# Optimization experiments

Hardware: AMD Instinct MI355X
Metric: run time of the kernel (lower is better)

Reference implementation:

```python
import jax, jax.numpy as jnp
import numpy as np

B, D, H = 65536, 3, 256  # collocation batch, coord dim, hidden width


def setup_inputs() -> dict:
    key = jax.random.key(0)
    ks = jax.random.split(key, 8)

    def init(k, shape, fan_in):
        return jax.random.normal(k, shape, dtype=jnp.float32) * np.float32(1.0 / np.sqrt(fan_in))

    return {
        "x": jax.random.uniform(ks[0], (B, D), dtype=jnp.float32, minval=0.1, maxval=1.0),
        "W0": init(ks[1], (D, H), D), "b0": jnp.zeros((H,), jnp.float32),
        "W1": init(ks[2], (H, H), H), "b1": jnp.zeros((H,), jnp.float32),
        "W2": init(ks[3], (H, H), H), "b2": jnp.zeros((H,), jnp.float32),
        "W3": init(ks[4], (H, H), H), "b3": jnp.zeros((H,), jnp.float32),
        "Wout": init(ks[5], (H, 1), H), "bout": jnp.zeros((1,), jnp.float32),
    }


def reference(x, W0, b0, W1, b1, W2, b2, W3, b3, Wout, bout):
    # Scalar PINN network u(xi), xi: [D]
    def u_fn(xi):
        h = jnp.tanh(xi @ W0 + b0)
        h = jnp.tanh(h @ W1 + b1)
        h = jnp.tanh(h @ W2 + b2)
        h = jnp.tanh(h @ W3 + b3)
        return (h @ Wout + bout)[0]

    u = jax.vmap(u_fn)(x)                               # [B]
    # batch_gradient: du/dx_i for every coordinate axis (Cartesian: no adjustment)
    grads = jax.vmap(jax.grad(u_fn))(x)                 # [B, D]
    # batch_hessian diagonal: d^2u/dx_i^2 via forward-over-reverse
    hess_fn = jax.jacfwd(jax.grad(u_fn))                # [D, D] per sample
    hess_diag = jax.vmap(lambda xi: jnp.diagonal(hess_fn(xi)))(x)  # [B, D]
    # pack (u, grad, hessian-diagonal) as the PDE-residual ingredients
    return jnp.concatenate([u[:, None], grads, hess_diag], axis=1)  # [B, 1+D+D]
```

## Files before the change

kernel.cpp:

```cpp
#include <hip/hip_runtime.h>
#include <hip/hip_fp16.h>

#define HDIM 256
#define MS 16
#define LDAK 264
#define CSTRIDE (MS * LDAK * 2)

typedef _Float16 half8 __attribute__((ext_vector_type(8)));
typedef _Float16 half4 __attribute__((ext_vector_type(4)));
typedef _Float16 half2v __attribute__((ext_vector_type(2)));
typedef float f32x4 __attribute__((ext_vector_type(4)));

__device__ __forceinline__ float fast_tanh(float x) {
    float e = __expf(2.0f * x);
    return 1.0f - 2.0f * __builtin_amdgcn_rcpf(e + 1.0f);
}

__device__ __forceinline__ half4 cvt4(float a, float b, float c, float d) {
    half2v lo = __builtin_bit_cast(half2v, __builtin_amdgcn_cvt_pkrtz(a, b));
    half2v hi = __builtin_bit_cast(half2v, __builtin_amdgcn_cvt_pkrtz(c, d));
    half4 r; r[0] = lo[0]; r[1] = lo[1]; r[2] = hi[0]; r[3] = hi[1];
    return r;
}

__device__ __forceinline__ void barrier_lds() {
    asm volatile("s_waitcnt lgkmcnt(0)\n\ts_barrier" ::: "memory");
}

__global__ __launch_bounds__(256) void pack_weights(const float* __restrict__ W1,
                                                    const float* __restrict__ W2,
                                                    const float* __restrict__ W3,
                                                    _Float16* __restrict__ out) {
    int tid = blockIdx.x * 256 + threadIdx.x;
    int l = tid >> 13;
    int idx = tid & 8191;
    int kg = idx >> 8;
    int n = idx & 255;
    const float* W = (l == 0) ? W1 : (l == 1) ? W2 : W3;
    half8 v;
    #pragma unroll
    for (int j = 0; j < 8; ++j) v[j] = (_Float16)W[(kg * 8 + j) * 256 + n];
    *(half8*)(out + l * 65536 + kg * 2048 + n * 8) = v;
}

__global__ __launch_bounds__(256, 2)
void pinn_fused(const float* __restrict__ x,
                const float* __restrict__ W0,
                const float* __restrict__ b0,
                const float* __restrict__ b1,
                const float* __restrict__ b2,
                const float* __restrict__ b3,
                const float* __restrict__ Wout,
                const float* __restrict__ bout,
                const _Float16* __restrict__ Wp,
                float* __restrict__ out) {
    __shared__ __align__(16) _Float16 Abuf[7 * MS][LDAK];
    __shared__ float part[4 * 7 * MS];

    const int tid  = threadIdx.x;
    const int lane = tid & 63;
    const int wid  = tid >> 6;
    const int qd   = lane >> 4;
    const int n15  = lane & 15;
    const int base = blockIdx.x * MS;
    const int nw   = wid * 64 + n15;

    const int voff0 = (qd * 256 + nw) * 8;

    const char* Ab = (const char*)Abuf;
    const int abase = (n15 * LDAK + qd * 8) * 2;
    char* Sb = (char*)Abuf;
    const int sbase = (n15 * LDAK + wid * 64 + qd * 4) * 2;

    const int perm[8] = {0, 2, 4, 6, 1, 3, 5, 7};

    half8 wf[3][4];

#define PREF(J) do { \
    if ((J) < 24) { \
        const int gp_ = (((J) >> 3) * 8) + perm[(J) & 7]; \
        _Pragma("unroll") \
        for (int t_ = 0; t_ < 4; ++t_) \
            wf[(J) % 3][t_] = *(const half8*)(Wp + gp_ * 8192 + voff0 + t_ * 128); \
    } \
} while (0)

#define KSTEP(ACC, J) do { \
    const int s_ = perm[(J) & 7]; \
    PREF((J) + 2); \
    half8 af_[7]; \
    _Pragma("unroll") \
    for (int c_ = 0; c_ < 7; ++c_) \
        af_[c_] = *(const half8*)(Ab + abase + c_ * CSTRIDE + s_ * 64); \
    _Pragma("unroll") \
    for (int c_ = 0; c_ < 7; ++c_) \
        _Pragma("unroll") \
        for (int t_ = 0; t_ < 4; ++t_) \
            ACC[c_][t_] = __builtin_amdgcn_mfma_f32_16x16x32_f16(wf[(J) % 3][t_], af_[c_], ACC[c_][t_], 0, 0, 0); \
} while (0)

#define ELEMW(ACC, BB, T) do { \
    const int ncol_ = wid * 64 + (T) * 16 + qd * 4; \
    f32x4 bv_ = *(const f32x4*)((BB) + ncol_); \
    float tv_[4], gj_[3][4], sj_[3][4]; \
    _Pragma("unroll") \
    for (int r_ = 0; r_ < 4; ++r_) { \
        float zv_ = ACC[0][T][r_] + bv_[r_]; \
        tv_[r_] = fast_tanh(zv_); \
        float dd_ = 1.f - tv_[r_] * tv_[r_]; \
        float c2_ = -2.f * tv_[r_] * dd_; \
        _Pragma("unroll") \
        for (int i_ = 0; i_ < 3; ++i_) { \
            float zg_ = ACC[1 + i_][T][r_]; \
            float zs_ = ACC[4 + i_][T][r_]; \
            gj_[i_][r_] = dd_ * zg_; \
            sj_[i_][r_] = dd_ * zs_ + c2_ * zg_ * zg_; \
        } \
    } \
    *(half4*)(Sb + sbase + 0 * CSTRIDE + (T) * 32) = cvt4(tv_[0], tv_[1], tv_[2], tv_[3]); \
    _Pragma("unroll") \
    for (int i_ = 0; i_ < 3; ++i_) { \
        *(half4*)(Sb + sbase + (1 + i_) * CSTRIDE + (T) * 32) = \
            cvt4(gj_[i_][0], gj_[i_][1], gj_[i_][2], gj_[i_][3]); \
        *(half4*)(Sb + sbase + (4 + i_) * CSTRIDE + (T) * 32) = \
            cvt4(sj_[i_][0], sj_[i_][1], sj_[i_][2], sj_[i_][3]); \
    } \
} while (0)

#define L0CHUNK(N0) do { \
    const int n0_ = (N0); \
    f32x4 w0v_[2], w1v_[2], w2v_[2], b0v_[2]; \
    w0v_[0] = *(const f32x4*)(W0 + n0_);            w0v_[1] = *(const f32x4*)(W0 + n0_ + 4); \
    w1v_[0] = *(const f32x4*)(W0 + HDIM + n0_);     w1v_[1] = *(const f32x4*)(W0 + HDIM + n0_ + 4); \
    w2v_[0] = *(const f32x4*)(W0 + 2 * HDIM + n0_); w2v_[1] = *(const f32x4*)(W0 + 2 * HDIM + n0_ + 4); \
    b0v_[0] = *(const f32x4*)(b0 + n0_);            b0v_[1] = *(const f32x4*)(b0 + n0_ + 4); \
    half8 h_[7]; \
    _Pragma("unroll") \
    for (int r_ = 0; r_ < 8; ++r_) { \
        const float w0_ = w0v_[r_ >> 2][r_ & 3]; \
        const float w1_ = w1v_[r_ >> 2][r_ & 3]; \
        const float w2_ = w2v_[r_ >> 2][r_ & 3]; \
        float z_  = x0 * w0_ + x1 * w1_ + x2 * w2_ + b0v_[r_ >> 2][r_ & 3]; \
        float tv_ = fast_tanh(z_); \
        float dd_ = 1.f - tv_ * tv_; \
        float c2_ = -2.f * tv_ * dd_; \
        h_[0][r_] = (_Float16)tv_; \
        h_[1][r_] = (_Float16)(dd_ * w0_); \
        h_[2][r_] = (_Float16)(dd_ * w1_); \
        h_[3][r_] = (_Float16)(dd_ * w2_); \
        h_[4][r_] = (_Float16)(c2_ * w0_ * w0_); \
        h_[5][r_] = (_Float16)(c2_ * w1_ * w1_); \
        h_[6][r_] = (_Float16)(c2_ * w2_ * w2_); \
    } \
    _Pragma("unroll") \
    for (int c_ = 0; c_ < 7; ++c_) \
        *(half8*)&Abuf[c_ * MS + m0][n0_] = h_[c_]; \
} while (0)

    PREF(0);
    PREF(1);

    const int m0 = tid & 15;
    const int cidx = tid >> 4;
    const int n0A = (cidx >> 2) * 64 + (cidx & 3) * 8;
    const float x0 = x[(base + m0) * 3 + 0];
    const float x1 = x[(base + m0) * 3 + 1];
    const float x2 = x[(base + m0) * 3 + 2];

    L0CHUNK(n0A);
    barrier_lds();

    f32x4 acc1[7][4];
    #pragma unroll
    for (int c = 0; c < 7; ++c)
        #pragma unroll
        for (int t = 0; t < 4; ++t) acc1[c][t] = (f32x4){0.f, 0.f, 0.f, 0.f};

    KSTEP(acc1, 0);
    L0CHUNK(n0A + 32);
    KSTEP(acc1, 1);
    KSTEP(acc1, 2);
    KSTEP(acc1, 3);
    barrier_lds();
    KSTEP(acc1, 4); KSTEP(acc1, 5); KSTEP(acc1, 6); KSTEP(acc1, 7);
    ELEMW(acc1, b1, 0);
    ELEMW(acc1, b1, 1);
    barrier_lds();

    f32x4 acc2[7][4];
    #pragma unroll
    for (int c = 0; c < 7; ++c)
        #pragma unroll
        for (int t = 0; t < 4; ++t) acc2[c][t] = (f32x4){0.f, 0.f, 0.f, 0.f};

    KSTEP(acc2, 8);
    ELEMW(acc1, b1, 2);
    KSTEP(acc2, 9);
    KSTEP(acc2, 10);
    ELEMW(acc1, b1, 3);
    KSTEP(acc2, 11);
    barrier_lds();
    KSTEP(acc2, 12); KSTEP(acc2, 13); KSTEP(acc2, 14); KSTEP(acc2, 15);
    ELEMW(acc2, b2, 0);
    ELEMW(acc2, b2, 1);
    barrier_lds();

    f32x4 acc3[7][4];
    #pragma unroll
    for (int c = 0; c < 7; ++c)
        #pragma unroll
        for (int t = 0; t < 4; ++t) acc3[c][t] = (f32x4){0.f, 0.f, 0.f, 0.f};

    KSTEP(acc3, 16);
    ELEMW(acc2, b2, 2);
    KSTEP(acc3, 17);
    KSTEP(acc3, 18);
    ELEMW(acc2, b2, 3);
    KSTEP(acc3, 19);
    barrier_lds();
    KSTEP(acc3, 20); KSTEP(acc3, 21); KSTEP(acc3, 22); KSTEP(acc3, 23);

    {
        float p[7] = {0.f, 0.f, 0.f, 0.f, 0.f, 0.f, 0.f};
        #pragma unroll
        for (int t = 0; t < 4; ++t) {
            const int ncol = wid * 64 + t * 16 + qd * 4;
            f32x4 bv = *(const f32x4*)(b3 + ncol);
            f32x4 wv = *(const f32x4*)(Wout + ncol);
            #pragma unroll
            for (int r = 0; r < 4; ++r) {
                float zv = acc3[0][t][r] + bv[r];
                float tv = fast_tanh(zv);
                float dd = 1.f - tv * tv;
                float c2 = -2.f * tv * dd;
                p[0] += tv * wv[r];
                #pragma unroll
                for (int i = 0; i < 3; ++i) {
                    float zg = acc3[1 + i][t][r];
                    float zs = acc3[4 + i][t][r];
                    p[1 + i] += (dd * zg) * wv[r];
                    p[4 + i] += (dd * zs + c2 * zg * zg) * wv[r];
                }
            }
        }
        #pragma unroll
        for (int c = 0; c < 7; ++c) {
            p[c] += __shfl_xor(p[c], 16, 64);
            p[c] += __shfl_xor(p[c], 32, 64);
        }
        if (lane < 16) {
            #pragma unroll
            for (int c = 0; c < 7; ++c)
                part[(wid * 7 + c) * MS + lane] = p[c];
        }
    }
    barrier_lds();

    if (tid < 7 * MS) {
        const int c = tid >> 4;
        const int m = tid & 15;
        float v = part[(0 * 7 + c) * MS + m] + part[(1 * 7 + c) * MS + m] +
                  part[(2 * 7 + c) * MS + m] + part[(3 * 7 + c) * MS + m];
        if (c == 0) v += bout[0];
        out[(base + m) * 7 + c] = v;
    }

#undef PREF
#undef KSTEP
#undef ELEMW
#undef L0CHUNK
}

extern "C" void kernel_launch(void* const* d_in, const int* in_sizes, int n_in,
                              void* d_out, int out_size, void* d_ws, size_t ws_size,
                              hipStream_t stream) {
    const float* xp   = (const float*)d_in[0];
    const float* W0   = (const float*)d_in[1];
    const float* b0   = (const float*)d_in[2];
    const float* W1   = (const float*)d_in[3];
    const float* b1   = (const float*)d_in[4];
    const float* W2   = (const float*)d_in[5];
    const float* b2   = (const float*)d_in[6];
    const float* W3   = (const float*)d_in[7];
    const float* b3   = (const float*)d_in[8];
    const float* Wout = (const float*)d_in[9];
    const float* bout = (const float*)d_in[10];
    _Float16* Wp = (_Float16*)d_ws;

    pack_weights<<<96, 256, 0, stream>>>(W1, W2, W3, Wp);
    pinn_fused<<<65536 / MS, 256, 0, stream>>>(xp, W0, b0, b1, b2, b3, Wout, bout, Wp,
                                               (float*)d_out);
}
```

Measured before the change: 251.4 us.

## Ping-pong two sample groups per block with 8 waves to overlap MFMA and elementwise

Each block now handles two 16-sample groups with 512 threads (8 waves, each owning 32 output columns), alternating the layer GEMMs of one group with the tanh/derivative elementwise work of the other across double LDS buffers. This is meant to hide the elementwise and LDS write phases behind MFMA work of the other group, and to halve per-wave accumulator registers. In exchange it doubles LDS use per block, removes the k-step permutation, and relies on the launch bounds still allowing enough occupancy.

```diff
diff --git a/kernel.cpp b/kernel.cpp
--- a/kernel.cpp
+++ b/kernel.cpp
@@ -43,7 +43,7 @@
     *(half8*)(out + l * 65536 + kg * 2048 + n * 8) = v;
 }
 
-__global__ __launch_bounds__(256, 2)
+__global__ __launch_bounds__(512, 2)
 void pinn_fused(const float* __restrict__ x,
                 const float* __restrict__ W0,
                 const float* __restrict__ b0,
@@ -54,53 +54,48 @@
                 const float* __restrict__ bout,
                 const _Float16* __restrict__ Wp,
                 float* __restrict__ out) {
-    __shared__ __align__(16) _Float16 Abuf[7 * MS][LDAK];
-    __shared__ float part[4 * 7 * MS];
+    __shared__ __align__(16) _Float16 AbA[7 * MS][LDAK];
+    __shared__ __align__(16) _Float16 AbB[7 * MS][LDAK];
+    __shared__ float part[2][8 * 7 * MS];
 
     const int tid  = threadIdx.x;
     const int lane = tid & 63;
     const int wid  = tid >> 6;
     const int qd   = lane >> 4;
     const int n15  = lane & 15;
-    const int base = blockIdx.x * MS;
-    const int nw   = wid * 64 + n15;
+    const int base = blockIdx.x * (2 * MS);
+    const int nw   = wid * 32 + n15;
 
     const int voff0 = (qd * 256 + nw) * 8;
-
-    const char* Ab = (const char*)Abuf;
     const int abase = (n15 * LDAK + qd * 8) * 2;
-    char* Sb = (char*)Abuf;
-    const int sbase = (n15 * LDAK + wid * 64 + qd * 4) * 2;
-
-    const int perm[8] = {0, 2, 4, 6, 1, 3, 5, 7};
-
-    half8 wf[3][4];
+    const int sbase = (n15 * LDAK + wid * 32 + qd * 4) * 2;
+
+    half8 wf[3][2];
 
 #define PREF(J) do { \
-    if ((J) < 24) { \
-        const int gp_ = (((J) >> 3) * 8) + perm[(J) & 7]; \
-        _Pragma("unroll") \
-        for (int t_ = 0; t_ < 4; ++t_) \
-            wf[(J) % 3][t_] = *(const half8*)(Wp + gp_ * 8192 + voff0 + t_ * 128); \
-    } \
-} while (0)
-
-#define KSTEP(ACC, J) do { \
-    const int s_ = perm[(J) & 7]; \
+    if ((J) < 48) { \
+        const int g_ = (((J) >> 4) * 8) + ((J) & 7); \
+        wf[(J) % 3][0] = *(const half8*)(Wp + g_ * 8192 + voff0); \
+        wf[(J) % 3][1] = *(const half8*)(Wp + g_ * 8192 + voff0 + 128); \
+    } \
+} while (0)
+
+#define KSTEP(ACC, AB, J) do { \
+    const int s_ = (J) & 7; \
     PREF((J) + 2); \
     half8 af_[7]; \
     _Pragma("unroll") \
     for (int c_ = 0; c_ < 7; ++c_) \
-        af_[c_] = *(const half8*)(Ab + abase + c_ * CSTRIDE + s_ * 64); \
+        af_[c_] = *(const half8*)((const char*)AB + abase + c_ * CSTRIDE + s_ * 64); \
     _Pragma("unroll") \
     for (int c_ = 0; c_ < 7; ++c_) \
         _Pragma("unroll") \
-        for (int t_ = 0; t_ < 4; ++t_) \
+        for (int t_ = 0; t_ < 2; ++t_) \
             ACC[c_][t_] = __builtin_amdgcn_mfma_f32_16x16x32_f16(wf[(J) % 3][t_], af_[c_], ACC[c_][t_], 0, 0, 0); \
 } while (0)
 
-#define ELEMW(ACC, BB, T) do { \
-    const int ncol_ = wid * 64 + (T) * 16 + qd * 4; \
+#define ELEMW(ACC, AB, BB, T) do { \
+    const int ncol_ = wid * 32 + (T) * 16 + qd * 4; \
     f32x4 bv_ = *(const f32x4*)((BB) + ncol_); \
     float tv_[4], gj_[3][4], sj_[3][4]; \
     _Pragma("unroll") \
@@ -117,30 +112,25 @@
             sj_[i_][r_] = dd_ * zs_ + c2_ * zg_ * zg_; \
         } \
     } \
-    *(half4*)(Sb + sbase + 0 * CSTRIDE + (T) * 32) = cvt4(tv_[0], tv_[1], tv_[2], tv_[3]); \
+    char* sb_ = (char*)AB + sbase; \
+    *(half4*)(sb_ + 0 * CSTRIDE + (T) * 32) = cvt4(tv_[0], tv_[1], tv_[2], tv_[3]); \
     _Pragma("unroll") \
     for (int i_ = 0; i_ < 3; ++i_) { \
-        *(half4*)(Sb + sbase + (1 + i_) * CSTRIDE + (T) * 32) = \
+        *(half4*)(sb_ + (1 + i_) * CSTRIDE + (T) * 32) = \
             cvt4(gj_[i_][0], gj_[i_][1], gj_[i_][2], gj_[i_][3]); \
-        *(half4*)(Sb + sbase + (4 + i_) * CSTRIDE + (T) * 32) = \
+        *(half4*)(sb_ + (4 + i_) * CSTRIDE + (T) * 32) = \
             cvt4(sj_[i_][0], sj_[i_][1], sj_[i_][2], sj_[i_][3]); \
     } \
 } while (0)
 
-#define L0CHUNK(N0) do { \
-    const int n0_ = (N0); \
-    f32x4 w0v_[2], w1v_[2], w2v_[2], b0v_[2]; \
-    w0v_[0] = *(const f32x4*)(W0 + n0_);            w0v_[1] = *(const f32x4*)(W0 + n0_ + 4); \
-    w1v_[0] = *(const f32x4*)(W0 + HDIM + n0_);     w1v_[1] = *(const f32x4*)(W0 + HDIM + n0_ + 4); \
-    w2v_[0] = *(const f32x4*)(W0 + 2 * HDIM + n0_); w2v_[1] = *(const f32x4*)(W0 + 2 * HDIM + n0_ + 4); \
-    b0v_[0] = *(const f32x4*)(b0 + n0_);            b0v_[1] = *(const f32x4*)(b0 + n0_ + 4); \
+#define L0G(AB, X0, X1, X2) do { \
     half8 h_[7]; \
     _Pragma("unroll") \
     for (int r_ = 0; r_ < 8; ++r_) { \
-        const float w0_ = w0v_[r_ >> 2][r_ & 3]; \
-        const float w1_ = w1v_[r_ >> 2][r_ & 3]; \
-        const float w2_ = w2v_[r_ >> 2][r_ & 3]; \
-        float z_  = x0 * w0_ + x1 * w1_ + x2 * w2_ + b0v_[r_ >> 2][r_ & 3]; \
+        const float w0_ = w0v[r_ >> 2][r_ & 3]; \
+        const float w1_ = w1v[r_ >> 2][r_ & 3]; \
+        const float w2_ = w2v[r_ >> 2][r_ & 3]; \
+        float z_  = (X0) * w0_ + (X1) * w1_ + (X2) * w2_ + b0v[r_ >> 2][r_ & 3]; \
         float tv_ = fast_tanh(z_); \
         float dd_ = 1.f - tv_ * tv_; \
         float c2_ = -2.f * tv_ * dd_; \
@@ -154,121 +144,139 @@
     } \
     _Pragma("unroll") \
     for (int c_ = 0; c_ < 7; ++c_) \
-        *(half8*)&Abuf[c_ * MS + m0][n0_] = h_[c_]; \
-} while (0)
+        *(half8*)&AB[c_ * MS + m0][n0] = h_[c_]; \
+} while (0)
+
+#define OUTG(ACC, G) do { \
+    float p_[7] = {0.f, 0.f, 0.f, 0.f, 0.f, 0.f, 0.f}; \
+    _Pragma("unroll") \
+    for (int t_ = 0; t_ < 2; ++t_) { \
+        const int ncol_ = wid * 32 + t_ * 16 + qd * 4; \
+        f32x4 bv_ = *(const f32x4*)(b3 + ncol_); \
+        f32x4 wv_ = *(const f32x4*)(Wout + ncol_); \
+        _Pragma("unroll") \
+        for (int r_ = 0; r_ < 4; ++r_) { \
+            float zv_ = ACC[0][t_][r_] + bv_[r_]; \
+            float tv_ = fast_tanh(zv_); \
+            float dd_ = 1.f - tv_ * tv_; \
+            float c2_ = -2.f * tv_ * dd_; \
+            p_[0] += tv_ * wv_[r_]; \
+            _Pragma("unroll") \
+            for (int i_ = 0; i_ < 3; ++i_) { \
+                float zg_ = ACC[1 + i_][t_][r_]; \
+                float zs_ = ACC[4 + i_][t_][r_]; \
+                p_[1 + i_] += (dd_ * zg_) * wv_[r_]; \
+                p_[4 + i_] += (dd_ * zs_ + c2_ * zg_ * zg_) * wv_[r_]; \
+            } \
+        } \
+    } \
+    _Pragma("unroll") \
+    for (int c_ = 0; c_ < 7; ++c_) { \
+        p_[c_] += __shfl_xor(p_[c_], 16, 64); \
+        p_[c_] += __shfl_xor(p_[c_], 32, 64); \
+    } \
+    if (lane < 16) { \
+        _Pragma("unroll") \
+        for (int c_ = 0; c_ < 7; ++c_) \
+            part[G][(wid * 7 + c_) * MS + lane] = p_[c_]; \
+    } \
+} while (0)
+
+#define ZACC(A_) do { \
+    _Pragma("unroll") \
+    for (int c_ = 0; c_ < 7; ++c_) \
+        _Pragma("unroll") \
+        for (int t_ = 0; t_ < 2; ++t_) A_[c_][t_] = (f32x4){0.f, 0.f, 0.f, 0.f}; \
+} while (0)
+
+    const int m0 = tid & 15;
+    const int n0 = (tid >> 4) * 8;
+    const float xa0 = x[(base + m0) * 3 + 0];
+    const float xa1 = x[(base + m0) * 3 + 1];
+    const float xa2 = x[(base + m0) * 3 + 2];
+    const float xb0 = x[(base + MS + m0) * 3 + 0];
+    const float xb1 = x[(base + MS + m0) * 3 + 1];
+    const float xb2 = x[(base + MS + m0) * 3 + 2];
 
     PREF(0);
     PREF(1);
 
-    const int m0 = tid & 15;
-    const int cidx = tid >> 4;
-    const int n0A = (cidx >> 2) * 64 + (cidx & 3) * 8;
-    const float x0 = x[(base + m0) * 3 + 0];
-    const float x1 = x[(base + m0) * 3 + 1];
-    const float x2 = x[(base + m0) * 3 + 2];
-
-    L0CHUNK(n0A);
-    barrier_lds();
-
-    f32x4 acc1[7][4];
-    #pragma unroll
-    for (int c = 0; c < 7; ++c)
+    f32x4 w0v[2], w1v[2], w2v[2], b0v[2];
+    w0v[0] = *(const f32x4*)(W0 + n0);            w0v[1] = *(const f32x4*)(W0 + n0 + 4);
+    w1v[0] = *(const f32x4*)(W0 + HDIM + n0);     w1v[1] = *(const f32x4*)(W0 + HDIM + n0 + 4);
+    w2v[0] = *(const f32x4*)(W0 + 2 * HDIM + n0); w2v[1] = *(const f32x4*)(W0 + 2 * HDIM + n0 + 4);
+    b0v[0] = *(const f32x4*)(b0 + n0);            b0v[1] = *(const f32x4*)(b0 + n0 + 4);
+
+    f32x4 accA[7][2], accB[7][2];
+
+    L0G(AbA, xa0, xa1, xa2);
+    barrier_lds();
+
+    ZACC(accA);
+    KSTEP(accA, AbA, 0);
+    KSTEP(accA, AbA, 1);
+    L0G(AbB, xb0, xb1, xb2);
+    KSTEP(accA, AbA, 2); KSTEP(accA, AbA, 3); KSTEP(accA, AbA, 4);
+    KSTEP(accA, AbA, 5); KSTEP(accA, AbA, 6); KSTEP(accA, AbA, 7);
+    barrier_lds();
+
+    ZACC(accB);
+    KSTEP(accB, AbB, 8);
+    ELEMW(accA, AbA, b1, 0);
+    KSTEP(accB, AbB, 9); KSTEP(accB, AbB, 10); KSTEP(accB, AbB, 11);
+    ELEMW(accA, AbA, b1, 1);
+    KSTEP(accB, AbB, 12); KSTEP(accB, AbB, 13); KSTEP(accB, AbB, 14); KSTEP(accB, AbB, 15);
+    barrier_lds();
+
+    ZACC(accA);
+    KSTEP(accA, AbA, 16);
+    ELEMW(accB, AbB, b1, 0);
+    KSTEP(accA, AbA, 17); KSTEP(accA, AbA, 18); KSTEP(accA, AbA, 19);
+    ELEMW(accB, AbB, b1, 1);
+    KSTEP(accA, AbA, 20); KSTEP(accA, AbA, 21); KSTEP(accA, AbA, 22); KSTEP(accA, AbA, 23);
+    barrier_lds();
+
+    ZACC(accB);
+    KSTEP(accB, AbB, 24);
+    ELEMW(accA, AbA, b2, 0);
+    KSTEP(accB, AbB, 25); KSTEP(accB, AbB, 26); KSTEP(accB, AbB, 27);
+    ELEMW(accA, AbA, b2, 1);
+    KSTEP(accB, AbB, 28); KSTEP(accB, AbB, 29); KSTEP(accB, AbB, 30); KSTEP(accB, AbB, 31);
+    barrier_lds();
+
+    ZACC(accA);
+    KSTEP(accA, AbA, 32);
+    ELEMW(accB, AbB, b2, 0);
+    KSTEP(accA, AbA, 33); KSTEP(accA, AbA, 34); KSTEP(accA, AbA, 35);
+    ELEMW(accB, AbB, b2, 1);
+    KSTEP(accA, AbA, 36); KSTEP(accA, AbA, 37); KSTEP(accA, AbA, 38); KSTEP(accA, AbA, 39);
+    barrier_lds();
+
+    ZACC(accB);
+    KSTEP(accB, AbB, 40); KSTEP(accB, AbB, 41);
+    OUTG(accA, 0);
+    KSTEP(accB, AbB, 42); KSTEP(accB, AbB, 43); KSTEP(accB, AbB, 44);
+    KSTEP(accB, AbB, 45); KSTEP(accB, AbB, 46); KSTEP(accB, AbB, 47);
+    OUTG(accB, 1);
+    barrier_lds();
+
+    if ((tid & 255) < 112) {
+        const int g = tid >> 8;
+        const int c = (tid & 255) >> 4;
+        const int m = tid & 15;
+        float v = 0.f;
         #pragma unroll
-        for (int t = 0; t < 4; ++t) acc1[c][t] = (f32x4){0.f, 0.f, 0.f, 0.f};
-
-    KSTEP(acc1, 0);
-    L0CHUNK(n0A + 32);
-    KSTEP(acc1, 1);
-    KSTEP(acc1, 2);
-    KSTEP(acc1, 3);
-    barrier_lds();
-    KSTEP(acc1, 4); KSTEP(acc1, 5); KSTEP(acc1, 6); KSTEP(acc1, 7);
-    ELEMW(acc1, b1, 0);
-    ELEMW(acc1, b1, 1);
-    barrier_lds();
-
-    f32x4 acc2[7][4];
-    #pragma unroll
-    for (int c = 0; c < 7; ++c)
-        #pragma unroll
-        for (int t = 0; t < 4; ++t) acc2[c][t] = (f32x4){0.f, 0.f, 0.f, 0.f};
-
-    KSTEP(acc2, 8);
-    ELEMW(acc1, b1, 2);
-    KSTEP(acc2, 9);
-    KSTEP(acc2, 10);
-    ELEMW(acc1, b1, 3);
-    KSTEP(acc2, 11);
-    barrier_lds();
-    KSTEP(acc2, 12); KSTEP(acc2, 13); KSTEP(acc2, 14); KSTEP(acc2, 15);
-    ELEMW(acc2, b2, 0);
-    ELEMW(acc2, b2, 1);
-    barrier_lds();
-
-    f32x4 acc3[7][4];
-    #pragma unroll
-    for (int c = 0; c < 7; ++c)
-        #pragma unroll
-        for (int t = 0; t < 4; ++t) acc3[c][t] = (f32x4){0.f, 0.f, 0.f, 0.f};
-
-    KSTEP(acc3, 16);
-    ELEMW(acc2, b2, 2);
-    KSTEP(acc3, 17);
-    KSTEP(acc3, 18);
-    ELEMW(acc2, b2, 3);
-    KSTEP(acc3, 19);
-    barrier_lds();
-    KSTEP(acc3, 20); KSTEP(acc3, 21); KSTEP(acc3, 22); KSTEP(acc3, 23);
-
-    {
-        float p[7] = {0.f, 0.f, 0.f, 0.f, 0.f, 0.f, 0.f};
-        #pragma unroll
-        for (int t = 0; t < 4; ++t) {
-            const int ncol = wid * 64 + t * 16 + qd * 4;
-            f32x4 bv = *(const f32x4*)(b3 + ncol);
-            f32x4 wv = *(const f32x4*)(Wout + ncol);
-            #pragma unroll
-            for (int r = 0; r < 4; ++r) {
-                float zv = acc3[0][t][r] + bv[r];
-                float tv = fast_tanh(zv);
-                float dd = 1.f - tv * tv;
-                float c2 = -2.f * tv * dd;
-                p[0] += tv * wv[r];
-                #pragma unroll
-                for (int i = 0; i < 3; ++i) {
-                    float zg = acc3[1 + i][t][r];
-                    float zs = acc3[4 + i][t][r];
-                    p[1 + i] += (dd * zg) * wv[r];
-                    p[4 + i] += (dd * zs + c2 * zg * zg) * wv[r];
-                }
-            }
-        }
-        #pragma unroll
-        for (int c = 0; c < 7; ++c) {
-            p[c] += __shfl_xor(p[c], 16, 64);
-            p[c] += __shfl_xor(p[c], 32, 64);
-        }
-        if (lane < 16) {
-            #pragma unroll
-            for (int c = 0; c < 7; ++c)
-                part[(wid * 7 + c) * MS + lane] = p[c];
-        }
-    }
-    barrier_lds();
-
-    if (tid < 7 * MS) {
-        const int c = tid >> 4;
-        const int m = tid & 15;
-        float v = part[(0 * 7 + c) * MS + m] + part[(1 * 7 + c) * MS + m] +
-                  part[(2 * 7 + c) * MS + m] + part[(3 * 7 + c) * MS + m];
+        for (int w = 0; w < 8; ++w) v += part[g][(w * 7 + c) * MS + m];
         if (c == 0) v += bout[0];
-        out[(base + m) * 7 + c] = v;
+        out[(base + g * MS + m) * 7 + c] = v;
     }
 
 #undef PREF
 #undef KSTEP
 #undef ELEMW
-#undef L0CHUNK
+#undef L0G
+#undef OUTG
+#undef ZACC
 }
 
 extern "C" void kernel_launch(void* const* d_in, const int* in_sizes, int n_in,
@@ -288,6 +296,6 @@
     _Float16* Wp = (_Float16*)d_ws;
 
     pack_weights<<<96, 256, 0, stream>>>(W1, W2, W3, Wp);
-    pinn_fused<<<65536 / MS, 256, 0, stream>>>(xp, W0, b0, b1, b2, b3, Wout, bout, Wp,
-                                               (float*)d_out);
-}
+    pinn_fused<<<65536 / (2 * MS), 512, 0, stream>>>(xp, W0, b0, b1, b2, b3, Wout, bout,
+                                                     Wp, (float*)d_out);
+}
```

After: 263.1 us. +4.7%, slower.
